# Kernel tuning notes

Hardware: AMD Instinct MI355X
Metric: run time of the kernel (lower is better)

Reference implementation:

```python
import jax, jax.numpy as jnp
import numpy as np

B, H, W, C = 64, 56, 56, 256
WS, SHIFT, HEADS = 7, 3, 8
N = WS * WS
HID = 4 * C


def _rel_pos_index():
    coords = np.stack(np.meshgrid(np.arange(WS), np.arange(WS), indexing='ij'))  # (2,ws,ws)
    flat = coords.reshape(2, -1)
    rel = (flat[:, :, None] - flat[:, None, :]).transpose(1, 2, 0)  # (N,N,2)
    rel[..., 0] += WS - 1
    rel[..., 1] += WS - 1
    rel[..., 0] *= 2 * WS - 1
    return rel.sum(-1)  # (N,N)


def _attn_mask():
    img = np.zeros((H, W), dtype=np.int32)
    cnt = 0
    for hs in (slice(0, -WS), slice(-WS, -SHIFT), slice(-SHIFT, None)):
        for ws_ in (slice(0, -WS), slice(-WS, -SHIFT), slice(-SHIFT, None)):
            img[hs, ws_] = cnt
            cnt += 1
    mw = img.reshape(H // WS, WS, W // WS, WS).transpose(0, 2, 1, 3).reshape(-1, N)  # (nW,N)
    diff = mw[:, None, :] - mw[:, :, None]
    return np.where(diff != 0, -100.0, 0.0).astype(np.float32)  # (nW,N,N)


def setup_inputs() -> dict:
    key = jax.random.key(0)
    ks = jax.random.split(key, 16)
    s = 0.02
    return {
        'x': jax.random.normal(ks[0], (B, H * W, C), jnp.float32),
        'norm1_g': jnp.ones((C,), jnp.float32),
        'norm1_b': jnp.zeros((C,), jnp.float32),
        'qkv_w': jax.random.normal(ks[1], (3 * C, C), jnp.float32) * s,
        'qkv_b': jnp.zeros((3 * C,), jnp.float32),
        'rpb_table': jax.random.normal(ks[2], ((2 * WS - 1) ** 2, HEADS), jnp.float32) * s,
        'proj_w': jax.random.normal(ks[3], (C, C), jnp.float32) * s,
        'proj_b': jnp.zeros((C,), jnp.float32),
        'norm2_g': jnp.ones((C,), jnp.float32),
        'norm2_b': jnp.zeros((C,), jnp.float32),
        'fc1_w': jax.random.normal(ks[4], (HID, C), jnp.float32) * s,
        'fc1_b': jnp.zeros((HID,), jnp.float32),
        'fc2_w': jax.random.normal(ks[5], (C, HID), jnp.float32) * s,
        'fc2_b': jnp.zeros((C,), jnp.float32),
        'rel_index': jnp.asarray(_rel_pos_index(), jnp.int32),
        'attn_mask': jnp.asarray(_attn_mask(), jnp.float32),
    }


def _ln(y, g, b):
    m = y.mean(-1, keepdims=True)
    v = ((y - m) ** 2).mean(-1, keepdims=True)
    return (y - m) / jnp.sqrt(v + 1e-5) * g + b


def reference(x, norm1_g, norm1_b, qkv_w, qkv_b, rpb_table, proj_w, proj_b,
              norm2_g, norm2_b, fc1_w, fc1_b, fc2_w, fc2_b, rel_index, attn_mask):
    Bx, L, Cx = x.shape
    shortcut = x
    y = _ln(x, norm1_g, norm1_b).reshape(Bx, H, W, Cx)
    # cyclic shift (roll_index_select equivalent)
    y = jnp.roll(y, (-SHIFT, -SHIFT), axis=(1, 2))
    # window partition -> (B*nW, N, C)
    y = y.reshape(Bx, H // WS, WS, W // WS, WS, Cx).transpose(0, 1, 3, 2, 4, 5).reshape(-1, N, Cx)
    B_ = y.shape[0]
    hd = Cx // HEADS
    qkv = (y @ qkv_w.T + qkv_b).reshape(B_, N, 3, HEADS, hd).transpose(2, 0, 3, 1, 4)
    q, k, v = qkv[0], qkv[1], qkv[2]
    scale = hd ** -0.5
    attn = jnp.einsum('bhnd,bhmd->bhnm', q * scale, k)  # (B_,H,N,N)
    rpb = rpb_table[rel_index.reshape(-1)].reshape(N, N, HEADS).transpose(2, 0, 1)
    attn = attn + rpb[None]
    nW = attn_mask.shape[0]
    attn = attn.reshape(B_ // nW, nW, HEADS, N, N) + attn_mask[None, :, None]
    attn = jax.nn.softmax(attn.reshape(B_, HEADS, N, N), axis=-1)
    o = jnp.einsum('bhnm,bhmd->bhnd', attn, v).transpose(0, 2, 1, 3).reshape(B_, N, Cx)
    o = o @ proj_w.T + proj_b
    # window reverse + reverse shift
    o = o.reshape(Bx, H // WS, W // WS, WS, WS, Cx).transpose(0, 1, 3, 2, 4, 5).reshape(Bx, H, W, Cx)
    o = jnp.roll(o, (SHIFT, SHIFT), axis=(1, 2)).reshape(Bx, L, Cx)
    x = shortcut + o  # drop_path prob = 0 / eval mode
    h = _ln(x, norm2_g, norm2_b)
    h = h @ fc1_w.T + fc1_b
    h = h * jax.nn.sigmoid(1.702 * h)  # fast_gelu
    h = h @ fc2_w.T + fc2_b
    return x + h
```

## Files before the change

kernel.cpp:

```cpp
#include <hip/hip_runtime.h>

typedef unsigned short u16;
typedef __attribute__((ext_vector_type(8))) short bf16x8;
typedef __attribute__((ext_vector_type(4))) float f32x4;

struct __align__(8) U16x4 { u16 x, y, z, w; };

__device__ __forceinline__ u16 f2bf(float f) {
  unsigned u = __float_as_uint(f);
  u = (u + 0x7FFFu + ((u >> 16) & 1u)) >> 16;
  return (u16)u;
}

__device__ __forceinline__ void gload16(const u16* g, u16* l) {
  __builtin_amdgcn_global_load_lds((const __attribute__((address_space(1))) void*)g,
                                   (__attribute__((address_space(3))) void*)l, 16, 0, 0);
}

#define MTOK 200704
#define CDIM 256
#define NC3  768
#define HIDD 1024

#define OFF_QKV   0UL
#define OFF_O     308281344UL
#define OFF_H1    0UL
#define OFF_Y     411041792UL
#define OFF_WQ    513802240UL
#define OFF_WP    514195456UL
#define OFF_W1    514326528UL
#define OFF_W2    514850816UL
#define OFF_RPB   515375104UL

__global__ __launch_bounds__(256) void prep_kernel(
    const float* __restrict__ qkv_w, const float* __restrict__ proj_w,
    const float* __restrict__ fc1_w, const float* __restrict__ fc2_w,
    const float* __restrict__ rpb_table, const int* __restrict__ rel_index,
    u16* wq, u16* wp, u16* w1, u16* w2, float* rpbf) {
  int i = blockIdx.x * 256 + threadIdx.x;
  if (i < 196608) { wq[i] = f2bf(qkv_w[i]); return; }
  int j = i - 196608;
  if (j < 65536) { wp[j] = f2bf(proj_w[j]); return; }
  int k = j - 65536;
  if (k < 262144) { w1[k] = f2bf(fc1_w[k]); return; }
  int l = k - 262144;
  if (l < 262144) { w2[l] = f2bf(fc2_w[l]); return; }
  int r = l - 262144;
  if (r < 8 * 2401) {
    int h = r / 2401, nm = r % 2401;
    rpbf[r] = rpb_table[rel_index[nm] * 8 + h];
  }
}

__global__ __launch_bounds__(256) void ln1_kernel(const float* __restrict__ x,
                                                  const float* __restrict__ gg,
                                                  const float* __restrict__ bb,
                                                  u16* __restrict__ y) {
  int wid = threadIdx.x >> 6, lane = threadIdx.x & 63;
  int m = blockIdx.x * 4 + wid;
  int win = m / 49, n = m % 49;
  int b = win >> 6, widx = win & 63;
  int hh = (widx >> 3) * 7 + n / 7 + 3; if (hh >= 56) hh -= 56;
  int ww = (widx & 7) * 7 + n % 7 + 3; if (ww >= 56) ww -= 56;
  const float* src = x + ((size_t)b * 3136 + hh * 56 + ww) * CDIM + lane * 4;
  float4 v = *(const float4*)src;
  float s = v.x + v.y + v.z + v.w;
  float s2 = v.x * v.x + v.y * v.y + v.z * v.z + v.w * v.w;
  for (int o = 32; o; o >>= 1) { s += __shfl_xor(s, o); s2 += __shfl_xor(s2, o); }
  float mean = s * (1.f / 256.f);
  float inv = rsqrtf(s2 * (1.f / 256.f) - mean * mean + 1e-5f);
  int c = lane * 4;
  float4 gv = *(const float4*)(gg + c);
  float4 bv = *(const float4*)(bb + c);
  U16x4 o4;
  o4.x = f2bf((v.x - mean) * inv * gv.x + bv.x);
  o4.y = f2bf((v.y - mean) * inv * gv.y + bv.y);
  o4.z = f2bf((v.z - mean) * inv * gv.z + bv.z);
  o4.w = f2bf((v.w - mean) * inv * gv.w + bv.w);
  *(U16x4*)(y + (size_t)m * CDIM + c) = o4;
}

__global__ __launch_bounds__(256) void ln2_kernel(const float* __restrict__ x2,
                                                  const float* __restrict__ gg,
                                                  const float* __restrict__ bb,
                                                  u16* __restrict__ y) {
  int wid = threadIdx.x >> 6, lane = threadIdx.x & 63;
  int m = blockIdx.x * 4 + wid;
  const float* src = x2 + (size_t)m * CDIM + lane * 4;
  float4 v = *(const float4*)src;
  float s = v.x + v.y + v.z + v.w;
  float s2 = v.x * v.x + v.y * v.y + v.z * v.z + v.w * v.w;
  for (int o = 32; o; o >>= 1) { s += __shfl_xor(s, o); s2 += __shfl_xor(s2, o); }
  float mean = s * (1.f / 256.f);
  float inv = rsqrtf(s2 * (1.f / 256.f) - mean * mean + 1e-5f);
  int c = lane * 4;
  float4 gv = *(const float4*)(gg + c);
  float4 bv = *(const float4*)(bb + c);
  U16x4 o4;
  o4.x = f2bf((v.x - mean) * inv * gv.x + bv.x);
  o4.y = f2bf((v.y - mean) * inv * gv.y + bv.y);
  o4.z = f2bf((v.z - mean) * inv * gv.z + bv.z);
  o4.w = f2bf((v.w - mean) * inv * gv.w + bv.w);
  *(U16x4*)(y + (size_t)m * CDIM + c) = o4;
}

template <int K>
__device__ __forceinline__ void gemm_tile(const u16* __restrict__ A, const u16* __restrict__ B,
                                          int m0, int n0, f32x4 acc[4][4], u16* lds) {
  const int tid = threadIdx.x;
  const int lane = tid & 63;
  const int lr = lane & 15, g = lane >> 4;
  const int wid = tid >> 6, wr = wid >> 1, wc = wid & 1;
  u16* lds_a = lds;
  u16* lds_b = lds + 4096;
  const int srow = tid >> 2, schunk = tid & 3;
  const u16* ga = A + (size_t)(m0 + srow) * K + schunk * 8;
  const u16* gb = B + (size_t)(n0 + srow) * K + schunk * 8;
  u16* la = lds_a + srow * 32 + schunk * 8;
  u16* lb = lds_b + srow * 32 + schunk * 8;

#pragma unroll 2
  for (int k0 = 0; k0 < K; k0 += 32) {
    gload16(ga + k0, la);
    gload16(ga + (size_t)64 * K + k0, la + 2048);
    gload16(gb + k0, lb);
    gload16(gb + (size_t)64 * K + k0, lb + 2048);
    __syncthreads();
    bf16x8 af[4], bfr[4];
#pragma unroll
    for (int i = 0; i < 4; ++i) {
      af[i]  = *(const bf16x8*)(lds_a + (wr * 64 + i * 16 + lr) * 32 + g * 8);
      bfr[i] = *(const bf16x8*)(lds_b + (wc * 64 + i * 16 + lr) * 32 + g * 8);
    }
#pragma unroll
    for (int i = 0; i < 4; ++i)
#pragma unroll
      for (int j = 0; j < 4; ++j)
        acc[i][j] = __builtin_amdgcn_mfma_f32_16x16x32_bf16(af[i], bfr[j], acc[i][j], 0, 0, 0);
    __syncthreads();
  }
}

__device__ __forceinline__ int xcd_swz(int bid, int nwg) {
  return (bid & 7) * (nwg >> 3) + (bid >> 3);
}

#define GEMM_PROLOG(NVAL, KVAL)                                            \
  __shared__ u16 lds[8192];                                                \
  const int NTX = (NVAL) / 128;                                            \
  int logical = xcd_swz(blockIdx.x, NTX * (MTOK / 128));                   \
  int m0 = (logical / NTX) * 128, n0 = (logical % NTX) * 128;              \
  f32x4 zero = {0.f, 0.f, 0.f, 0.f};                                       \
  f32x4 acc[4][4] = {{zero, zero, zero, zero}, {zero, zero, zero, zero},   \
                     {zero, zero, zero, zero}, {zero, zero, zero, zero}};  \
  gemm_tile<KVAL>(A, B, m0, n0, acc, lds);                                 \
  const int lane = threadIdx.x & 63;                                       \
  const int lr = lane & 15, g = lane >> 4;                                 \
  const int wid = threadIdx.x >> 6, wr = wid >> 1, wc = wid & 1;

__global__ __launch_bounds__(256) void gemm_qkv(const u16* __restrict__ A, const u16* __restrict__ B,
                                                const float* __restrict__ bias, u16* __restrict__ out) {
  GEMM_PROLOG(NC3, 256)
#pragma unroll
  for (int i = 0; i < 4; ++i) {
    int row = m0 + wr * 64 + i * 16 + g * 4;
#pragma unroll
    for (int j = 0; j < 4; ++j) {
      int col = n0 + wc * 64 + j * 16 + lr;
      float bv = bias[col];
#pragma unroll
      for (int r = 0; r < 4; ++r)
        out[(size_t)(row + r) * NC3 + col] = f2bf(acc[i][j][r] + bv);
    }
  }
}

__global__ __launch_bounds__(256) void gemm_proj(const u16* __restrict__ A, const u16* __restrict__ B,
                                                 const float* __restrict__ bias,
                                                 const float* __restrict__ x, float* __restrict__ x2) {
  GEMM_PROLOG(CDIM, 256)
#pragma unroll
  for (int i = 0; i < 4; ++i) {
#pragma unroll
    for (int r = 0; r < 4; ++r) {
      int row = m0 + wr * 64 + i * 16 + g * 4 + r;
      int win = row / 49, n = row % 49;
      int b = win >> 6, widx = win & 63;
      int hh = (widx >> 3) * 7 + n / 7 + 3; if (hh >= 56) hh -= 56;
      int ww = (widx & 7) * 7 + n % 7 + 3; if (ww >= 56) ww -= 56;
      size_t dst = ((size_t)b * 3136 + hh * 56 + ww) * CDIM;
#pragma unroll
      for (int j = 0; j < 4; ++j) {
        int col = n0 + wc * 64 + j * 16 + lr;
        x2[dst + col] = x[dst + col] + acc[i][j][r] + bias[col];
      }
    }
  }
}

__global__ __launch_bounds__(256) void gemm_fc1(const u16* __restrict__ A, const u16* __restrict__ B,
                                                const float* __restrict__ bias, u16* __restrict__ out) {
  GEMM_PROLOG(HIDD, 256)
#pragma unroll
  for (int i = 0; i < 4; ++i) {
    int row = m0 + wr * 64 + i * 16 + g * 4;
#pragma unroll
    for (int j = 0; j < 4; ++j) {
      int col = n0 + wc * 64 + j * 16 + lr;
      float bv = bias[col];
#pragma unroll
      for (int r = 0; r < 4; ++r) {
        float v = acc[i][j][r] + bv;
        v = v / (1.f + __expf(-1.702f * v));
        out[(size_t)(row + r) * HIDD + col] = f2bf(v);
      }
    }
  }
}

__global__ __launch_bounds__(256) void gemm_fc2(const u16* __restrict__ A, const u16* __restrict__ B,
                                                const float* __restrict__ bias, float* __restrict__ out) {
  GEMM_PROLOG(CDIM, 1024)
#pragma unroll
  for (int i = 0; i < 4; ++i) {
    int row = m0 + wr * 64 + i * 16 + g * 4;
#pragma unroll
    for (int j = 0; j < 4; ++j) {
      int col = n0 + wc * 64 + j * 16 + lr;
      float bv = bias[col];
#pragma unroll
      for (int r = 0; r < 4; ++r) {
        size_t idx = (size_t)(row + r) * CDIM + col;
        out[idx] = out[idx] + acc[i][j][r] + bv;
      }
    }
  }
}

__global__ __launch_bounds__(256) void attn_kernel(const u16* __restrict__ qkv,
                                                   const float* __restrict__ rpbf,
                                                   const float* __restrict__ mask,
                                                   u16* __restrict__ o) {
  __shared__ u16 p_lds[4][64][72];
  const int lane = threadIdx.x & 63, wid = threadIdx.x >> 6;
  const int lr = lane & 15, g = lane >> 4;
  const int win = blockIdx.x >> 1;
  const int head = (blockIdx.x & 1) * 4 + wid;
  const int widx = win & 63;
  const size_t base = (size_t)win * 49 * NC3 + head * 32;

  bf16x8 aq[4], bk[4];
#pragma unroll
  for (int R = 0; R < 4; ++R) {
    int n = R * 16 + lr; if (n > 48) n = 48;
    aq[R] = *(const bf16x8*)(qkv + base + (size_t)n * NC3 + 8 * g);
  }
#pragma unroll
  for (int Cc = 0; Cc < 4; ++Cc) {
    int mi = Cc * 16 + lr; if (mi > 48) mi = 48;
    bk[Cc] = *(const bf16x8*)(qkv + base + 256 + (size_t)mi * NC3 + 8 * g);
  }
  f32x4 zero = {0.f, 0.f, 0.f, 0.f};
  f32x4 s[4][4] = {{zero, zero, zero, zero}, {zero, zero, zero, zero},
                   {zero, zero, zero, zero}, {zero, zero, zero, zero}};
#pragma unroll
  for (int R = 0; R < 4; ++R)
#pragma unroll
    for (int Cc = 0; Cc < 4; ++Cc)
      s[R][Cc] = __builtin_amdgcn_mfma_f32_16x16x32_bf16(aq[R], bk[Cc], s[R][Cc], 0, 0, 0);

  const float scale = 0.17677669529663687f;
  const float* rpb_h = rpbf + head * 2401;
  const float* msk = mask + widx * 2401;
#pragma unroll
  for (int R = 0; R < 4; ++R) {
#pragma unroll
    for (int reg = 0; reg < 4; ++reg) {
      int n = R * 16 + g * 4 + reg;
      float mx = -1e30f;
#pragma unroll
      for (int Cc = 0; Cc < 4; ++Cc) {
        int mc = Cc * 16 + lr;
        float v;
        if (mc < 49)
          v = (n < 49) ? s[R][Cc][reg] * scale + rpb_h[n * 49 + mc] + msk[n * 49 + mc] : 0.f;
        else
          v = -1e30f;
        s[R][Cc][reg] = v;
        mx = fmaxf(mx, v);
      }
#pragma unroll
      for (int o_ = 1; o_ < 16; o_ <<= 1) mx = fmaxf(mx, __shfl_xor(mx, o_));
      float sum = 0.f;
#pragma unroll
      for (int Cc = 0; Cc < 4; ++Cc) {
        float p = __expf(s[R][Cc][reg] - mx);
        s[R][Cc][reg] = p;
        sum += p;
      }
#pragma unroll
      for (int o_ = 1; o_ < 16; o_ <<= 1) sum += __shfl_xor(sum, o_);
      float rs = 1.f / sum;
      int rowi = R * 16 + g * 4 + reg;
#pragma unroll
      for (int Cc = 0; Cc < 4; ++Cc) {
        int mc = Cc * 16 + lr;
        p_lds[wid][rowi][mc] = f2bf(s[R][Cc][reg] * rs);
      }
    }
  }
  __syncthreads();

  f32x4 oacc[4][2] = {{zero, zero}, {zero, zero}, {zero, zero}, {zero, zero}};
  const u16* vbase = qkv + base + 512;
#pragma unroll
  for (int ks = 0; ks < 2; ++ks) {
    bf16x8 bv[2];
#pragma unroll
    for (int D = 0; D < 2; ++D) {
#pragma unroll
      for (int i = 0; i < 8; ++i) {
        int mi = ks * 32 + 8 * g + i; if (mi > 48) mi = 48;
        bv[D][i] = (short)vbase[(size_t)mi * NC3 + D * 16 + lr];
      }
    }
#pragma unroll
    for (int R = 0; R < 4; ++R) {
      bf16x8 ap = *(const bf16x8*)(&p_lds[wid][R * 16 + lr][ks * 32 + 8 * g]);
      oacc[R][0] = __builtin_amdgcn_mfma_f32_16x16x32_bf16(ap, bv[0], oacc[R][0], 0, 0, 0);
      oacc[R][1] = __builtin_amdgcn_mfma_f32_16x16x32_bf16(ap, bv[1], oacc[R][1], 0, 0, 0);
    }
  }
#pragma unroll
  for (int R = 0; R < 4; ++R)
#pragma unroll
    for (int D = 0; D < 2; ++D)
#pragma unroll
      for (int reg = 0; reg < 4; ++reg) {
        int n = R * 16 + g * 4 + reg;
        if (n < 49)
          o[((size_t)win * 49 + n) * CDIM + head * 32 + D * 16 + lr] = f2bf(oacc[R][D][reg]);
      }
}

extern "C" void kernel_launch(void* const* d_in, const int* in_sizes, int n_in,
                              void* d_out, int out_size, void* d_ws, size_t ws_size,
                              hipStream_t stream) {
  const float* x      = (const float*)d_in[0];
  const float* n1g    = (const float*)d_in[1];
  const float* n1b    = (const float*)d_in[2];
  const float* qkv_w  = (const float*)d_in[3];
  const float* qkv_b  = (const float*)d_in[4];
  const float* rpb_t  = (const float*)d_in[5];
  const float* proj_w = (const float*)d_in[6];
  const float* proj_b = (const float*)d_in[7];
  const float* n2g    = (const float*)d_in[8];
  const float* n2b    = (const float*)d_in[9];
  const float* fc1_w  = (const float*)d_in[10];
  const float* fc1_b  = (const float*)d_in[11];
  const float* fc2_w  = (const float*)d_in[12];
  const float* fc2_b  = (const float*)d_in[13];
  const int*   relidx = (const int*)d_in[14];
  const float* amask  = (const float*)d_in[15];
  float* out = (float*)d_out;
  char* ws = (char*)d_ws;

  u16* qkv_buf = (u16*)(ws + OFF_QKV);
  u16* o_buf   = (u16*)(ws + OFF_O);
  u16* h1_buf  = (u16*)(ws + OFF_H1);
  u16* y_buf   = (u16*)(ws + OFF_Y);
  u16* wq = (u16*)(ws + OFF_WQ);
  u16* wp = (u16*)(ws + OFF_WP);
  u16* w1 = (u16*)(ws + OFF_W1);
  u16* w2 = (u16*)(ws + OFF_W2);
  float* rpbf = (float*)(ws + OFF_RPB);

  prep_kernel<<<3148, 256, 0, stream>>>(qkv_w, proj_w, fc1_w, fc2_w, rpb_t, relidx, wq, wp, w1, w2, rpbf);
  ln1_kernel<<<MTOK / 4, 256, 0, stream>>>(x, n1g, n1b, y_buf);
  gemm_qkv<<<(NC3 / 128) * (MTOK / 128), 256, 0, stream>>>(y_buf, wq, qkv_b, qkv_buf);
  attn_kernel<<<4096 * 2, 256, 0, stream>>>(qkv_buf, rpbf, amask, o_buf);
  gemm_proj<<<(CDIM / 128) * (MTOK / 128), 256, 0, stream>>>(o_buf, wp, proj_b, x, out);
  ln2_kernel<<<MTOK / 4, 256, 0, stream>>>(out, n2g, n2b, y_buf);
  gemm_fc1<<<(HIDD / 128) * (MTOK / 128), 256, 0, stream>>>(y_buf, w1, fc1_b, h1_buf);
  gemm_fc2<<<(CDIM / 128) * (MTOK / 128), 256, 0, stream>>>(h1_buf, w2, fc2_b, out);
}
```

Baseline: 1.415 ms.

## Double-buffer GEMM LDS with XOR swizzle and transpose MFMA outputs for vector stores

The shared GEMM tile now uses two LDS buffers so the global-to-LDS load of the next K slice overlaps the MFMAs on the current one. LDS rows get an XOR swizzle to cut bank conflicts. MFMA operands are swapped in the GEMMs and in attention so each lane holds four consecutive columns, which lets the epilogues and softmax write with 4-wide vector stores and shortens the row reductions to two shuffles. LDS use per block doubles, which may lower occupancy.

```diff
diff --git a/kernel.cpp b/kernel.cpp
--- a/kernel.cpp
+++ b/kernel.cpp
@@ -110,33 +110,45 @@
   const int tid = threadIdx.x;
   const int lane = tid & 63;
   const int lr = lane & 15, g = lane >> 4;
-  const int wid = tid >> 6, wr = wid >> 1, wc = wid & 1;
-  u16* lds_a = lds;
-  u16* lds_b = lds + 4096;
-  const int srow = tid >> 2, schunk = tid & 3;
+  const int wr = (tid >> 6) >> 1, wc = (tid >> 6) & 1;
+  const int srow = tid >> 2;
+  const int schunk = (tid & 3) ^ ((tid >> 3) & 3);
   const u16* ga = A + (size_t)(m0 + srow) * K + schunk * 8;
   const u16* gb = B + (size_t)(n0 + srow) * K + schunk * 8;
-  u16* la = lds_a + srow * 32 + schunk * 8;
-  u16* lb = lds_b + srow * 32 + schunk * 8;
-
-#pragma unroll 2
-  for (int k0 = 0; k0 < K; k0 += 32) {
+  const int swz = (g ^ ((lr >> 1) & 3)) * 8;
+
+  auto STAGE = [&](int bsel, int k0) {
+    u16* la = lds + bsel * 8192 + tid * 8;
     gload16(ga + k0, la);
     gload16(ga + (size_t)64 * K + k0, la + 2048);
-    gload16(gb + k0, lb);
-    gload16(gb + (size_t)64 * K + k0, lb + 2048);
+    gload16(gb + k0, la + 4096);
+    gload16(gb + (size_t)64 * K + k0, la + 6144);
+  };
+  auto COMPUTE = [&](int bsel) {
+    const u16* ba = lds + bsel * 8192;
+    const u16* bb = ba + 4096;
+    bf16x8 af[4], bfr[4];
+#pragma unroll
+    for (int i = 0; i < 4; ++i) {
+      af[i]  = *(const bf16x8*)(ba + (wr * 64 + i * 16 + lr) * 32 + swz);
+      bfr[i] = *(const bf16x8*)(bb + (wc * 64 + i * 16 + lr) * 32 + swz);
+    }
+#pragma unroll
+    for (int i = 0; i < 4; ++i)
+#pragma unroll
+      for (int j = 0; j < 4; ++j)
+        acc[i][j] = __builtin_amdgcn_mfma_f32_16x16x32_bf16(bfr[j], af[i], acc[i][j], 0, 0, 0);
+  };
+
+  constexpr int NT = K / 32;
+  STAGE(0, 0);
+  __syncthreads();
+  for (int t = 0; t < NT; t += 2) {
+    if (t + 1 < NT) STAGE(1, (t + 1) * 32);
+    COMPUTE(0);
     __syncthreads();
-    bf16x8 af[4], bfr[4];
-#pragma unroll
-    for (int i = 0; i < 4; ++i) {
-      af[i]  = *(const bf16x8*)(lds_a + (wr * 64 + i * 16 + lr) * 32 + g * 8);
-      bfr[i] = *(const bf16x8*)(lds_b + (wc * 64 + i * 16 + lr) * 32 + g * 8);
-    }
-#pragma unroll
-    for (int i = 0; i < 4; ++i)
-#pragma unroll
-      for (int j = 0; j < 4; ++j)
-        acc[i][j] = __builtin_amdgcn_mfma_f32_16x16x32_bf16(af[i], bfr[j], acc[i][j], 0, 0, 0);
+    if (t + 2 < NT) STAGE(0, (t + 2) * 32);
+    COMPUTE(1);
     __syncthreads();
   }
 }
@@ -146,7 +158,7 @@
 }
 
 #define GEMM_PROLOG(NVAL, KVAL)                                            \
-  __shared__ u16 lds[8192];                                                \
+  __shared__ u16 lds[16384];                                               \
   const int NTX = (NVAL) / 128;                                            \
   int logical = xcd_swz(blockIdx.x, NTX * (MTOK / 128));                   \
   int m0 = (logical / NTX) * 128, n0 = (logical % NTX) * 128;              \
@@ -163,14 +175,16 @@
   GEMM_PROLOG(NC3, 256)
 #pragma unroll
   for (int i = 0; i < 4; ++i) {
-    int row = m0 + wr * 64 + i * 16 + g * 4;
+    int row = m0 + wr * 64 + i * 16 + lr;
 #pragma unroll
     for (int j = 0; j < 4; ++j) {
-      int col = n0 + wc * 64 + j * 16 + lr;
-      float bv = bias[col];
-#pragma unroll
-      for (int r = 0; r < 4; ++r)
-        out[(size_t)(row + r) * NC3 + col] = f2bf(acc[i][j][r] + bv);
+      int cb = n0 + wc * 64 + j * 16 + g * 4;
+      U16x4 o4;
+      o4.x = f2bf(acc[i][j][0] + bias[cb + 0]);
+      o4.y = f2bf(acc[i][j][1] + bias[cb + 1]);
+      o4.z = f2bf(acc[i][j][2] + bias[cb + 2]);
+      o4.w = f2bf(acc[i][j][3] + bias[cb + 3]);
+      *(U16x4*)(out + (size_t)row * NC3 + cb) = o4;
     }
   }
 }
@@ -181,19 +195,23 @@
   GEMM_PROLOG(CDIM, 256)
 #pragma unroll
   for (int i = 0; i < 4; ++i) {
-#pragma unroll
-    for (int r = 0; r < 4; ++r) {
-      int row = m0 + wr * 64 + i * 16 + g * 4 + r;
-      int win = row / 49, n = row % 49;
-      int b = win >> 6, widx = win & 63;
-      int hh = (widx >> 3) * 7 + n / 7 + 3; if (hh >= 56) hh -= 56;
-      int ww = (widx & 7) * 7 + n % 7 + 3; if (ww >= 56) ww -= 56;
-      size_t dst = ((size_t)b * 3136 + hh * 56 + ww) * CDIM;
-#pragma unroll
-      for (int j = 0; j < 4; ++j) {
-        int col = n0 + wc * 64 + j * 16 + lr;
-        x2[dst + col] = x[dst + col] + acc[i][j][r] + bias[col];
-      }
+    int row = m0 + wr * 64 + i * 16 + lr;
+    int win = row / 49, n = row % 49;
+    int b = win >> 6, widx = win & 63;
+    int hh = (widx >> 3) * 7 + n / 7 + 3; if (hh >= 56) hh -= 56;
+    int ww = (widx & 7) * 7 + n % 7 + 3; if (ww >= 56) ww -= 56;
+    size_t dst = ((size_t)b * 3136 + hh * 56 + ww) * CDIM;
+#pragma unroll
+    for (int j = 0; j < 4; ++j) {
+      int cb = n0 + wc * 64 + j * 16 + g * 4;
+      float4 xv = *(const float4*)(x + dst + cb);
+      float4 bv = *(const float4*)(bias + cb);
+      float4 o4;
+      o4.x = xv.x + acc[i][j][0] + bv.x;
+      o4.y = xv.y + acc[i][j][1] + bv.y;
+      o4.z = xv.z + acc[i][j][2] + bv.z;
+      o4.w = xv.w + acc[i][j][3] + bv.w;
+      *(float4*)(x2 + dst + cb) = o4;
     }
   }
 }
@@ -203,17 +221,19 @@
   GEMM_PROLOG(HIDD, 256)
 #pragma unroll
   for (int i = 0; i < 4; ++i) {
-    int row = m0 + wr * 64 + i * 16 + g * 4;
+    int row = m0 + wr * 64 + i * 16 + lr;
 #pragma unroll
     for (int j = 0; j < 4; ++j) {
-      int col = n0 + wc * 64 + j * 16 + lr;
-      float bv = bias[col];
-#pragma unroll
-      for (int r = 0; r < 4; ++r) {
-        float v = acc[i][j][r] + bv;
-        v = v / (1.f + __expf(-1.702f * v));
-        out[(size_t)(row + r) * HIDD + col] = f2bf(v);
-      }
+      int cb = n0 + wc * 64 + j * 16 + g * 4;
+      float4 bv = *(const float4*)(bias + cb);
+      float v0 = acc[i][j][0] + bv.x, v1 = acc[i][j][1] + bv.y;
+      float v2 = acc[i][j][2] + bv.z, v3 = acc[i][j][3] + bv.w;
+      v0 = v0 / (1.f + __expf(-1.702f * v0));
+      v1 = v1 / (1.f + __expf(-1.702f * v1));
+      v2 = v2 / (1.f + __expf(-1.702f * v2));
+      v3 = v3 / (1.f + __expf(-1.702f * v3));
+      U16x4 o4 = {f2bf(v0), f2bf(v1), f2bf(v2), f2bf(v3)};
+      *(U16x4*)(out + (size_t)row * HIDD + cb) = o4;
     }
   }
 }
@@ -223,16 +243,18 @@
   GEMM_PROLOG(CDIM, 1024)
 #pragma unroll
   for (int i = 0; i < 4; ++i) {
-    int row = m0 + wr * 64 + i * 16 + g * 4;
+    int row = m0 + wr * 64 + i * 16 + lr;
 #pragma unroll
     for (int j = 0; j < 4; ++j) {
-      int col = n0 + wc * 64 + j * 16 + lr;
-      float bv = bias[col];
-#pragma unroll
-      for (int r = 0; r < 4; ++r) {
-        size_t idx = (size_t)(row + r) * CDIM + col;
-        out[idx] = out[idx] + acc[i][j][r] + bv;
-      }
+      int cb = n0 + wc * 64 + j * 16 + g * 4;
+      float* p = out + (size_t)row * CDIM + cb;
+      float4 ov = *(const float4*)p;
+      float4 bv = *(const float4*)(bias + cb);
+      ov.x += acc[i][j][0] + bv.x;
+      ov.y += acc[i][j][1] + bv.y;
+      ov.z += acc[i][j][2] + bv.z;
+      ov.w += acc[i][j][3] + bv.w;
+      *(float4*)p = ov;
     }
   }
 }
@@ -267,46 +289,48 @@
   for (int R = 0; R < 4; ++R)
 #pragma unroll
     for (int Cc = 0; Cc < 4; ++Cc)
-      s[R][Cc] = __builtin_amdgcn_mfma_f32_16x16x32_bf16(aq[R], bk[Cc], s[R][Cc], 0, 0, 0);
+      s[R][Cc] = __builtin_amdgcn_mfma_f32_16x16x32_bf16(bk[Cc], aq[R], s[R][Cc], 0, 0, 0);
 
   const float scale = 0.17677669529663687f;
   const float* rpb_h = rpbf + head * 2401;
   const float* msk = mask + widx * 2401;
 #pragma unroll
   for (int R = 0; R < 4; ++R) {
-#pragma unroll
-    for (int reg = 0; reg < 4; ++reg) {
-      int n = R * 16 + g * 4 + reg;
-      float mx = -1e30f;
-#pragma unroll
-      for (int Cc = 0; Cc < 4; ++Cc) {
-        int mc = Cc * 16 + lr;
-        float v;
-        if (mc < 49)
-          v = (n < 49) ? s[R][Cc][reg] * scale + rpb_h[n * 49 + mc] + msk[n * 49 + mc] : 0.f;
-        else
-          v = -1e30f;
+    int n = R * 16 + lr;
+    bool nok = n < 49;
+    int rbase = n * 49;
+    float mx = -1e30f;
+#pragma unroll
+    for (int Cc = 0; Cc < 4; ++Cc)
+#pragma unroll
+      for (int reg = 0; reg < 4; ++reg) {
+        int mc = Cc * 16 + g * 4 + reg;
+        float v = (nok && mc < 49)
+                    ? s[R][Cc][reg] * scale + rpb_h[rbase + mc] + msk[rbase + mc]
+                    : -1e30f;
         s[R][Cc][reg] = v;
         mx = fmaxf(mx, v);
       }
-#pragma unroll
-      for (int o_ = 1; o_ < 16; o_ <<= 1) mx = fmaxf(mx, __shfl_xor(mx, o_));
-      float sum = 0.f;
-#pragma unroll
-      for (int Cc = 0; Cc < 4; ++Cc) {
+    mx = fmaxf(mx, __shfl_xor(mx, 16));
+    mx = fmaxf(mx, __shfl_xor(mx, 32));
+    float sum = 0.f;
+#pragma unroll
+    for (int Cc = 0; Cc < 4; ++Cc)
+#pragma unroll
+      for (int reg = 0; reg < 4; ++reg) {
         float p = __expf(s[R][Cc][reg] - mx);
         s[R][Cc][reg] = p;
         sum += p;
       }
-#pragma unroll
-      for (int o_ = 1; o_ < 16; o_ <<= 1) sum += __shfl_xor(sum, o_);
-      float rs = 1.f / sum;
-      int rowi = R * 16 + g * 4 + reg;
-#pragma unroll
-      for (int Cc = 0; Cc < 4; ++Cc) {
-        int mc = Cc * 16 + lr;
-        p_lds[wid][rowi][mc] = f2bf(s[R][Cc][reg] * rs);
-      }
+    sum += __shfl_xor(sum, 16);
+    sum += __shfl_xor(sum, 32);
+    float rs = 1.f / sum;
+    int rowi = R * 16 + lr;
+#pragma unroll
+    for (int Cc = 0; Cc < 4; ++Cc) {
+      U16x4 p4 = {f2bf(s[R][Cc][0] * rs), f2bf(s[R][Cc][1] * rs),
+                  f2bf(s[R][Cc][2] * rs), f2bf(s[R][Cc][3] * rs)};
+      *(U16x4*)(&p_lds[wid][rowi][Cc * 16 + g * 4]) = p4;
     }
   }
   __syncthreads();
@@ -327,20 +351,22 @@
 #pragma unroll
     for (int R = 0; R < 4; ++R) {
       bf16x8 ap = *(const bf16x8*)(&p_lds[wid][R * 16 + lr][ks * 32 + 8 * g]);
-      oacc[R][0] = __builtin_amdgcn_mfma_f32_16x16x32_bf16(ap, bv[0], oacc[R][0], 0, 0, 0);
-      oacc[R][1] = __builtin_amdgcn_mfma_f32_16x16x32_bf16(ap, bv[1], oacc[R][1], 0, 0, 0);
-    }
-  }
-#pragma unroll
-  for (int R = 0; R < 4; ++R)
-#pragma unroll
-    for (int D = 0; D < 2; ++D)
-#pragma unroll
-      for (int reg = 0; reg < 4; ++reg) {
-        int n = R * 16 + g * 4 + reg;
-        if (n < 49)
-          o[((size_t)win * 49 + n) * CDIM + head * 32 + D * 16 + lr] = f2bf(oacc[R][D][reg]);
+      oacc[R][0] = __builtin_amdgcn_mfma_f32_16x16x32_bf16(bv[0], ap, oacc[R][0], 0, 0, 0);
+      oacc[R][1] = __builtin_amdgcn_mfma_f32_16x16x32_bf16(bv[1], ap, oacc[R][1], 0, 0, 0);
+    }
+  }
+#pragma unroll
+  for (int R = 0; R < 4; ++R) {
+    int n = R * 16 + lr;
+    if (n < 49) {
+#pragma unroll
+      for (int D = 0; D < 2; ++D) {
+        U16x4 o4 = {f2bf(oacc[R][D][0]), f2bf(oacc[R][D][1]),
+                    f2bf(oacc[R][D][2]), f2bf(oacc[R][D][3])};
+        *(U16x4*)(o + ((size_t)win * 49 + n) * CDIM + head * 32 + D * 16 + g * 4) = o4;
       }
+    }
+  }
 }
 
 extern "C" void kernel_launch(void* const* d_in, const int* in_sizes, int n_in,
```

Result: faster. 1.352 ms (-4.4%).
